# Optimization experiments

Hardware: AMD Instinct MI355X
Metric: run time of the kernel (lower is better)

Reference implementation:

```python
import jax, jax.numpy as jnp
import numpy as np

BOX_SIZE = 3  # box_counting default
ALPHA = 0.1
BETA = 0.01
RESOLUTION_FACTOR = 2


def _box_count_mean(p):
    """Mean over boxes of (#nonzero elements per box of BOX_SIZE in flattened p).
    Trailing remainder elements are dropped, matching num_boxes = len // box_size."""
    flat = jnp.abs(p.reshape(-1))
    nb = flat.shape[0] // BOX_SIZE
    counts = jnp.sum((flat[: nb * BOX_SIZE].reshape(nb, BOX_SIZE) > 0).astype(jnp.float32), axis=1)
    return jnp.mean(counts)


def setup_inputs() -> dict:
    key = jax.random.key(0)
    k1, k2 = jax.random.split(key)
    W1 = jax.random.normal(k1, (4096, 8192), dtype=jnp.float32)
    W2 = jax.random.normal(k2, (8192, 4096), dtype=jnp.float32)
    lambda_l1 = jnp.asarray(0.1, dtype=jnp.float32)  # learnable nn.Parameter
    return {"W1": W1, "W2": W2, "lambda_l1": lambda_l1, "epoch": 5, "total_epochs": 100}


def reference(W1, W2, lambda_l1, epoch, total_epochs):
    progress = 1.0 - epoch / total_epochs
    adjusted_alpha = ALPHA * progress
    adjusted_beta = BETA * progress
    fractal_loss = jnp.asarray(0.0, jnp.float32)
    multi_resolution_loss = jnp.asarray(0.0, jnp.float32)
    # Faithful to the original accumulation: the running fractal_loss is
    # re-multiplied by lambda_l1 after each parameter is added.
    for p in (W1, W2):
        fractal_loss = (fractal_loss + jnp.sum(jnp.abs(p)) ** 2) * lambda_l1
        # box counts were built via .item() into a fresh tensor -> detached
        multi_resolution_loss = multi_resolution_loss + jax.lax.stop_gradient(_box_count_mean(p)) ** RESOLUTION_FACTOR
    return adjusted_alpha * fractal_loss + adjusted_beta * multi_resolution_loss
```

## Files before the change

kernel.cpp:

```cpp
#include <hip/hip_runtime.h>

#define BLK 256
#define NBLOCKS 2048

typedef float floatx4 __attribute__((ext_vector_type(4)));

__inline__ __device__ float waveReduceSumF(float v) {
    #pragma unroll
    for (int o = 32; o > 0; o >>= 1) v += __shfl_down(v, o, 64);
    return v;
}
__inline__ __device__ unsigned int waveReduceSumU(unsigned int v) {
    #pragma unroll
    for (int o = 32; o > 0; o >>= 1) v += __shfl_down(v, o, 64);
    return v;
}

__global__ __launch_bounds__(BLK) void frac_reduce2_kernel(
    const float* __restrict__ x1, long long n1, long long nc1,
    const float* __restrict__ x2, long long n2, long long nc2,
    float* __restrict__ psum1, unsigned int* __restrict__ pcnt1,
    float* __restrict__ psum2, unsigned int* __restrict__ pcnt2)
{
    const long long stride = (long long)gridDim.x * blockDim.x;
    const long long tid0   = (long long)blockIdx.x * blockDim.x + threadIdx.x;

    float s1 = 0.f, s2 = 0.f;
    unsigned int c1 = 0u, c2 = 0u;

    {
        const long long nvec = n1 >> 2;
        const floatx4* __restrict__ xv = (const floatx4*)x1;
        for (long long i = tid0; i < nvec; i += stride) {
            floatx4 v = __builtin_nontemporal_load(&xv[i]);
            float ax = fabsf(v.x), ay = fabsf(v.y), az = fabsf(v.z), aw = fabsf(v.w);
            s1 += (ax + ay) + (az + aw);
            long long base = i << 2;
            c1 += (ax > 0.f && base + 0 < nc1);
            c1 += (ay > 0.f && base + 1 < nc1);
            c1 += (az > 0.f && base + 2 < nc1);
            c1 += (aw > 0.f && base + 3 < nc1);
        }
    }
    {
        const long long nvec = n2 >> 2;
        const floatx4* __restrict__ xv = (const floatx4*)x2;
        for (long long i = tid0; i < nvec; i += stride) {
            floatx4 v = __builtin_nontemporal_load(&xv[i]);
            float ax = fabsf(v.x), ay = fabsf(v.y), az = fabsf(v.z), aw = fabsf(v.w);
            s2 += (ax + ay) + (az + aw);
            long long base = i << 2;
            c2 += (ax > 0.f && base + 0 < nc2);
            c2 += (ay > 0.f && base + 1 < nc2);
            c2 += (az > 0.f && base + 2 < nc2);
            c2 += (aw > 0.f && base + 3 < nc2);
        }
    }

    s1 = waveReduceSumF(s1); s2 = waveReduceSumF(s2);
    c1 = waveReduceSumU(c1); c2 = waveReduceSumU(c2);
    __shared__ float ls1[BLK / 64], ls2[BLK / 64];
    __shared__ unsigned int lc1[BLK / 64], lc2[BLK / 64];
    int lane = threadIdx.x & 63;
    int wid  = threadIdx.x >> 6;
    if (lane == 0) { ls1[wid] = s1; ls2[wid] = s2; lc1[wid] = c1; lc2[wid] = c2; }
    __syncthreads();
    if (wid == 0) {
        float fs1 = (lane < BLK / 64) ? ls1[lane] : 0.f;
        float fs2 = (lane < BLK / 64) ? ls2[lane] : 0.f;
        unsigned int fc1 = (lane < BLK / 64) ? lc1[lane] : 0u;
        unsigned int fc2 = (lane < BLK / 64) ? lc2[lane] : 0u;
        fs1 = waveReduceSumF(fs1); fs2 = waveReduceSumF(fs2);
        fc1 = waveReduceSumU(fc1); fc2 = waveReduceSumU(fc2);
        if (lane == 0) {
            psum1[blockIdx.x] = fs1; pcnt1[blockIdx.x] = fc1;
            psum2[blockIdx.x] = fs2; pcnt2[blockIdx.x] = fc2;
        }
    }
}

__global__ __launch_bounds__(BLK) void frac_final_kernel(
    const float* __restrict__ psum1, const unsigned int* __restrict__ pcnt1,
    const float* __restrict__ psum2, const unsigned int* __restrict__ pcnt2,
    int nblocks,
    const float* __restrict__ lambda_p,
    const int* __restrict__ epoch_p,
    const int* __restrict__ total_p,
    long long nb1, long long nb2,
    float* __restrict__ out)
{
    float s1 = 0.f, s2 = 0.f;
    unsigned int c1 = 0u, c2 = 0u;
    for (int i = threadIdx.x; i < nblocks; i += blockDim.x) {
        s1 += psum1[i]; c1 += pcnt1[i];
        s2 += psum2[i]; c2 += pcnt2[i];
    }
    s1 = waveReduceSumF(s1); s2 = waveReduceSumF(s2);
    c1 = waveReduceSumU(c1); c2 = waveReduceSumU(c2);
    __shared__ float ls1[BLK / 64], ls2[BLK / 64];
    __shared__ unsigned int lc1[BLK / 64], lc2[BLK / 64];
    int lane = threadIdx.x & 63;
    int wid  = threadIdx.x >> 6;
    if (lane == 0) { ls1[wid] = s1; ls2[wid] = s2; lc1[wid] = c1; lc2[wid] = c2; }
    __syncthreads();
    if (threadIdx.x == 0) {
        float S1 = 0.f, S2 = 0.f;
        unsigned long long C1 = 0ull, C2 = 0ull;
        #pragma unroll
        for (int w = 0; w < BLK / 64; ++w) {
            S1 += ls1[w]; S2 += ls2[w]; C1 += lc1[w]; C2 += lc2[w];
        }
        float lam = *lambda_p;
        float progress = 1.0f - (float)(*epoch_p) / (float)(*total_p);
        float adj_alpha = 0.1f  * progress;
        float adj_beta  = 0.01f * progress;

        float fractal = (S1 * S1) * lam;
        fractal = (fractal + S2 * S2) * lam;

        float m1 = (float)((double)C1 / (double)nb1);
        float m2 = (float)((double)C2 / (double)nb2);
        float mrl = m1 * m1 + m2 * m2;

        *out = adj_alpha * fractal + adj_beta * mrl;
    }
}

extern "C" void kernel_launch(void* const* d_in, const int* in_sizes, int n_in,
                              void* d_out, int out_size, void* d_ws, size_t ws_size,
                              hipStream_t stream) {
    const float* W1       = (const float*)d_in[0];
    const float* W2       = (const float*)d_in[1];
    const float* lambda_p = (const float*)d_in[2];
    const int*   epoch_p  = (const int*)d_in[3];
    const int*   total_p  = (const int*)d_in[4];
    float* out = (float*)d_out;

    long long n1 = (long long)in_sizes[0];
    long long n2 = (long long)in_sizes[1];
    long long nb1 = n1 / 3, nb2 = n2 / 3;

    float* psum1 = (float*)d_ws;
    float* psum2 = psum1 + NBLOCKS;
    unsigned int* pcnt1 = (unsigned int*)(psum2 + NBLOCKS);
    unsigned int* pcnt2 = pcnt1 + NBLOCKS;

    frac_reduce2_kernel<<<NBLOCKS, BLK, 0, stream>>>(
        W1, n1, nb1 * 3, W2, n2, nb2 * 3, psum1, pcnt1, psum2, pcnt2);
    frac_final_kernel<<<1, BLK, 0, stream>>>(psum1, pcnt1, psum2, pcnt2, NBLOCKS,
                                             lambda_p, epoch_p, total_p,
                                             nb1, nb2, out);
}
```

Baseline: 47.48 us.

## Fuse final reduction into main kernel via last-block atomic ticket

Merges the two-kernel reduction into one kernel. Each block writes its partial sums and takes an atomic ticket, and the last block performs the final reduction and computes the loss. The per-element index bounds checks in the hot loop are replaced by a scalar tail correction done once at the end. This removes one kernel launch and the per-element compare work, but adds a memset launch for the counter, threadfences and a serial tail fix-up.

```diff
diff --git a/kernel.cpp b/kernel.cpp
--- a/kernel.cpp
+++ b/kernel.cpp
@@ -16,11 +16,16 @@
     return v;
 }
 
-__global__ __launch_bounds__(BLK) void frac_reduce2_kernel(
+__global__ __launch_bounds__(BLK) void frac_fused_kernel(
     const float* __restrict__ x1, long long n1, long long nc1,
     const float* __restrict__ x2, long long n2, long long nc2,
-    float* __restrict__ psum1, unsigned int* __restrict__ pcnt1,
-    float* __restrict__ psum2, unsigned int* __restrict__ pcnt2)
+    const float* __restrict__ lambda_p,
+    const int* __restrict__ epoch_p,
+    const int* __restrict__ total_p,
+    float* psum1, unsigned int* pcnt1,
+    float* psum2, unsigned int* pcnt2,
+    unsigned int* counter,
+    float* out)
 {
     const long long stride = (long long)gridDim.x * blockDim.x;
     const long long tid0   = (long long)blockIdx.x * blockDim.x + threadIdx.x;
@@ -30,30 +35,24 @@
 
     {
         const long long nvec = n1 >> 2;
-        const floatx4* __restrict__ xv = (const floatx4*)x1;
+        const floatx4* xv = (const floatx4*)x1;
         for (long long i = tid0; i < nvec; i += stride) {
             floatx4 v = __builtin_nontemporal_load(&xv[i]);
             float ax = fabsf(v.x), ay = fabsf(v.y), az = fabsf(v.z), aw = fabsf(v.w);
             s1 += (ax + ay) + (az + aw);
-            long long base = i << 2;
-            c1 += (ax > 0.f && base + 0 < nc1);
-            c1 += (ay > 0.f && base + 1 < nc1);
-            c1 += (az > 0.f && base + 2 < nc1);
-            c1 += (aw > 0.f && base + 3 < nc1);
+            c1 += (unsigned int)(ax > 0.f) + (unsigned int)(ay > 0.f)
+                + (unsigned int)(az > 0.f) + (unsigned int)(aw > 0.f);
         }
     }
     {
         const long long nvec = n2 >> 2;
-        const floatx4* __restrict__ xv = (const floatx4*)x2;
+        const floatx4* xv = (const floatx4*)x2;
         for (long long i = tid0; i < nvec; i += stride) {
             floatx4 v = __builtin_nontemporal_load(&xv[i]);
             float ax = fabsf(v.x), ay = fabsf(v.y), az = fabsf(v.z), aw = fabsf(v.w);
             s2 += (ax + ay) + (az + aw);
-            long long base = i << 2;
-            c2 += (ax > 0.f && base + 0 < nc2);
-            c2 += (ay > 0.f && base + 1 < nc2);
-            c2 += (az > 0.f && base + 2 < nc2);
-            c2 += (aw > 0.f && base + 3 < nc2);
+            c2 += (unsigned int)(ax > 0.f) + (unsigned int)(ay > 0.f)
+                + (unsigned int)(az > 0.f) + (unsigned int)(aw > 0.f);
         }
     }
 
@@ -61,55 +60,67 @@
     c1 = waveReduceSumU(c1); c2 = waveReduceSumU(c2);
     __shared__ float ls1[BLK / 64], ls2[BLK / 64];
     __shared__ unsigned int lc1[BLK / 64], lc2[BLK / 64];
-    int lane = threadIdx.x & 63;
-    int wid  = threadIdx.x >> 6;
-    if (lane == 0) { ls1[wid] = s1; ls2[wid] = s2; lc1[wid] = c1; lc2[wid] = c2; }
-    __syncthreads();
-    if (wid == 0) {
-        float fs1 = (lane < BLK / 64) ? ls1[lane] : 0.f;
-        float fs2 = (lane < BLK / 64) ? ls2[lane] : 0.f;
-        unsigned int fc1 = (lane < BLK / 64) ? lc1[lane] : 0u;
-        unsigned int fc2 = (lane < BLK / 64) ? lc2[lane] : 0u;
-        fs1 = waveReduceSumF(fs1); fs2 = waveReduceSumF(fs2);
-        fc1 = waveReduceSumU(fc1); fc2 = waveReduceSumU(fc2);
-        if (lane == 0) {
-            psum1[blockIdx.x] = fs1; pcnt1[blockIdx.x] = fc1;
-            psum2[blockIdx.x] = fs2; pcnt2[blockIdx.x] = fc2;
-        }
-    }
-}
-
-__global__ __launch_bounds__(BLK) void frac_final_kernel(
-    const float* __restrict__ psum1, const unsigned int* __restrict__ pcnt1,
-    const float* __restrict__ psum2, const unsigned int* __restrict__ pcnt2,
-    int nblocks,
-    const float* __restrict__ lambda_p,
-    const int* __restrict__ epoch_p,
-    const int* __restrict__ total_p,
-    long long nb1, long long nb2,
-    float* __restrict__ out)
-{
-    float s1 = 0.f, s2 = 0.f;
-    unsigned int c1 = 0u, c2 = 0u;
-    for (int i = threadIdx.x; i < nblocks; i += blockDim.x) {
-        s1 += psum1[i]; c1 += pcnt1[i];
-        s2 += psum2[i]; c2 += pcnt2[i];
-    }
-    s1 = waveReduceSumF(s1); s2 = waveReduceSumF(s2);
-    c1 = waveReduceSumU(c1); c2 = waveReduceSumU(c2);
-    __shared__ float ls1[BLK / 64], ls2[BLK / 64];
-    __shared__ unsigned int lc1[BLK / 64], lc2[BLK / 64];
+    __shared__ unsigned int sTicket;
     int lane = threadIdx.x & 63;
     int wid  = threadIdx.x >> 6;
     if (lane == 0) { ls1[wid] = s1; ls2[wid] = s2; lc1[wid] = c1; lc2[wid] = c2; }
     __syncthreads();
     if (threadIdx.x == 0) {
-        float S1 = 0.f, S2 = 0.f;
-        unsigned long long C1 = 0ull, C2 = 0ull;
+        float bs1 = 0.f, bs2 = 0.f;
+        unsigned int bc1 = 0u, bc2 = 0u;
         #pragma unroll
         for (int w = 0; w < BLK / 64; ++w) {
-            S1 += ls1[w]; S2 += ls2[w]; C1 += lc1[w]; C2 += lc2[w];
+            bs1 += ls1[w]; bs2 += ls2[w]; bc1 += lc1[w]; bc2 += lc2[w];
         }
+        psum1[blockIdx.x] = bs1; pcnt1[blockIdx.x] = bc1;
+        psum2[blockIdx.x] = bs2; pcnt2[blockIdx.x] = bc2;
+        __threadfence();
+        sTicket = atomicAdd(counter, 1u);
+    }
+    __syncthreads();
+    if (sTicket != (unsigned int)(gridDim.x - 1)) return;
+
+    __threadfence();
+    volatile float* vp1 = psum1;  volatile float* vp2 = psum2;
+    volatile unsigned int* vc1 = pcnt1;  volatile unsigned int* vc2 = pcnt2;
+
+    float fs1 = 0.f, fs2 = 0.f;
+    unsigned int fc1 = 0u, fc2 = 0u;
+    for (int i = threadIdx.x; i < NBLOCKS; i += BLK) {
+        fs1 += vp1[i]; fc1 += vc1[i];
+        fs2 += vp2[i]; fc2 += vc2[i];
+    }
+    fs1 = waveReduceSumF(fs1); fs2 = waveReduceSumF(fs2);
+    fc1 = waveReduceSumU(fc1); fc2 = waveReduceSumU(fc2);
+    __syncthreads();
+    if (lane == 0) { ls1[wid] = fs1; ls2[wid] = fs2; lc1[wid] = fc1; lc2[wid] = fc2; }
+    __syncthreads();
+    if (threadIdx.x == 0) {
+        float S1 = 0.f, S2 = 0.f;
+        long long C1 = 0, C2 = 0;
+        #pragma unroll
+        for (int w = 0; w < BLK / 64; ++w) {
+            S1 += ls1[w]; S2 += ls2[w]; C1 += (long long)lc1[w]; C2 += (long long)lc2[w];
+        }
+        {
+            long long v4 = (n1 >> 2) << 2;
+            for (long long j = v4; j < n1; ++j) {
+                float a = fabsf(x1[j]);
+                S1 += a;
+                if (j < nc1 && a > 0.f) C1++;
+            }
+            for (long long j = nc1; j < v4; ++j)
+                if (fabsf(x1[j]) > 0.f) C1--;
+            long long w4 = (n2 >> 2) << 2;
+            for (long long j = w4; j < n2; ++j) {
+                float a = fabsf(x2[j]);
+                S2 += a;
+                if (j < nc2 && a > 0.f) C2++;
+            }
+            for (long long j = nc2; j < w4; ++j)
+                if (fabsf(x2[j]) > 0.f) C2--;
+        }
+
         float lam = *lambda_p;
         float progress = 1.0f - (float)(*epoch_p) / (float)(*total_p);
         float adj_alpha = 0.1f  * progress;
@@ -118,8 +129,8 @@
         float fractal = (S1 * S1) * lam;
         fractal = (fractal + S2 * S2) * lam;
 
-        float m1 = (float)((double)C1 / (double)nb1);
-        float m2 = (float)((double)C2 / (double)nb2);
+        float m1 = (float)((double)C1 / (double)(nc1 / 3));
+        float m2 = (float)((double)C2 / (double)(nc2 / 3));
         float mrl = m1 * m1 + m2 * m2;
 
         *out = adj_alpha * fractal + adj_beta * mrl;
@@ -138,16 +149,18 @@
 
     long long n1 = (long long)in_sizes[0];
     long long n2 = (long long)in_sizes[1];
-    long long nb1 = n1 / 3, nb2 = n2 / 3;
+    long long nc1 = (n1 / 3) * 3, nc2 = (n2 / 3) * 3;
 
     float* psum1 = (float*)d_ws;
     float* psum2 = psum1 + NBLOCKS;
     unsigned int* pcnt1 = (unsigned int*)(psum2 + NBLOCKS);
     unsigned int* pcnt2 = pcnt1 + NBLOCKS;
+    unsigned int* counter = pcnt2 + NBLOCKS;
 
-    frac_reduce2_kernel<<<NBLOCKS, BLK, 0, stream>>>(
-        W1, n1, nb1 * 3, W2, n2, nb2 * 3, psum1, pcnt1, psum2, pcnt2);
-    frac_final_kernel<<<1, BLK, 0, stream>>>(psum1, pcnt1, psum2, pcnt2, NBLOCKS,
-                                             lambda_p, epoch_p, total_p,
-                                             nb1, nb2, out);
+    hipMemsetAsync(counter, 0, sizeof(unsigned int), stream);
+
+    frac_fused_kernel<<<NBLOCKS, BLK, 0, stream>>>(
+        W1, n1, nc1, W2, n2, nc2,
+        lambda_p, epoch_p, total_p,
+        psum1, pcnt1, psum2, pcnt2, counter, out);
 }
```

Result: slower. 129.3 us (+172.4%).
